# Kernel tuning notes

Measured on AMD Instinct MI355X. Metric: run time of the kernel, lower is better.

The kernel has to match this reference:

```python
import jax, jax.numpy as jnp
import numpy as np
from jax.ops import segment_sum

N_NODES = 100000
N_EDGES = 3200000
NUM_FEATURES = 256


def setup_inputs() -> dict:
    key = jax.random.key(0)
    ks = jax.random.split(key, 12)
    def lin(k, fan_in, fan_out):
        bound = 1.0 / np.sqrt(fan_in)
        kw, kb = jax.random.split(k)
        W = jax.random.uniform(kw, (fan_in, fan_out), jnp.float32, -bound, bound)
        b = jax.random.uniform(kb, (fan_out,), jnp.float32, -bound, bound)
        return W, b
    x = jax.random.normal(ks[0], (N_NODES, NUM_FEATURES), jnp.float32)
    edge_index = jax.random.randint(ks[1], (2, N_EDGES), 0, N_NODES, jnp.int64 if jax.config.jax_enable_x64 else jnp.int32)
    W1, b1 = lin(ks[2], NUM_FEATURES, 64)
    W2, b2 = lin(ks[3], 64, 32)
    W3, b3 = lin(ks[4], 32, 16)
    Ws02, bs02 = lin(ks[5], NUM_FEATURES, 32)
    Ws03, bs03 = lin(ks[6], NUM_FEATURES, 16)
    Ws13, bs13 = lin(ks[7], 64, 16)
    Wout, bout = lin(ks[8], 16, 1)
    return dict(x=x, edge_index=edge_index, W1=W1, b1=b1, W2=W2, b2=b2,
                W3=W3, b3=b3, Ws02=Ws02, bs02=bs02, Ws03=Ws03, bs03=bs03,
                Ws13=Ws13, bs13=bs13, Wout=Wout, bout=bout)


def _deg_inv_sqrt(edge_index, n_nodes):
    # gcn_norm with self-loops: degree counted at target nodes, +1 for self-loop
    dst = edge_index[1]
    deg = segment_sum(jnp.ones(edge_index.shape[1], jnp.float32), dst, num_segments=n_nodes) + 1.0
    return jnp.where(deg > 0, jax.lax.rsqrt(deg), 0.0)


def _gcn_conv(x, W, b, edge_index, dinv):
    # PyG GCNConv: h = x W; out[i] = sum_{j->i} dinv[j]*dinv[i]*h[j] + dinv[i]^2*h[i] + b
    src, dst = edge_index[0], edge_index[1]
    h = x @ W                                   # [N, out]
    norm = (dinv[src] * dinv[dst])[:, None]     # [E, 1]
    agg = segment_sum(h[src] * norm, dst, num_segments=x.shape[0])
    agg = agg + (dinv * dinv)[:, None] * h      # self-loop term
    return agg + b


def reference(x, edge_index, W1, b1, W2, b2, W3, b3,
              Ws02, bs02, Ws03, bs03, Ws13, bs13, Wout, bout):
    # Dropout in eval mode (identity).
    dinv = _deg_inv_sqrt(edge_index, x.shape[0])
    x1 = jax.nn.relu(_gcn_conv(x, W1, b1, edge_index, dinv))
    x2 = jax.nn.relu(_gcn_conv(x1, W2, b2, edge_index, dinv) + x @ Ws02 + bs02)
    x3 = jax.nn.relu(_gcn_conv(x2, W3, b3, edge_index, dinv)
                     + x @ Ws03 + bs03 + x1 @ Ws13 + bs13)
    return jax.nn.sigmoid(x3 @ Wout + bout)
```

## Files before the change

### kernel.cpp

```cpp
#include <hip/hip_runtime.h>
#include <hip/hip_bf16.h>
#include <math.h>


#define NBUCK_MAX 512
#define P1_CHUNK 8192
#define EPT 32
#define BCAP 9216

typedef __attribute__((ext_vector_type(8))) short bfrag;
typedef __attribute__((ext_vector_type(4))) float f4_t;
typedef __attribute__((ext_vector_type(2))) float f2_t;

__device__ inline float uaf(unsigned u) { return __uint_as_float(u); }
__device__ inline ushort f2bf(float f) {
    __hip_bfloat16 b = __float2bfloat16(f);
    return *reinterpret_cast<ushort*>(&b);
}
__device__ inline bfrag cvt8(const float4 a, const float4 b) {
    union { ushort u[8]; bfrag f; } r;
    r.u[0] = f2bf(a.x); r.u[1] = f2bf(a.y); r.u[2] = f2bf(a.z); r.u[3] = f2bf(a.w);
    r.u[4] = f2bf(b.x); r.u[5] = f2bf(b.y); r.u[6] = f2bf(b.z); r.u[7] = f2bf(b.w);
    return r.f;
}
__device__ inline bfrag ld_bfrag(const ushort* p) {
    const uint4 raw = *reinterpret_cast<const uint4*>(p);
    return *reinterpret_cast<const bfrag*>(&raw);
}


__global__ __launch_bounds__(256) void bucket_hist_kernel(
    const int* __restrict__ dst, int E, int* __restrict__ bucket_count, int nbuckets)
{
    __shared__ int lhist[NBUCK_MAX];
    for (int i = threadIdx.x; i < nbuckets; i += 256) lhist[i] = 0;
    __syncthreads();
    const int stride = gridDim.x * 256;
    for (int e = blockIdx.x * 256 + threadIdx.x; e < E; e += stride)
        atomicAdd(&lhist[dst[e] >> 8], 1);
    __syncthreads();
    for (int i = threadIdx.x; i < nbuckets; i += 256) {
        int c = lhist[i];
        if (c) atomicAdd(&bucket_count[i], c);
    }
}

__global__ __launch_bounds__(512) void bucket_scan_kernel(
    const int* __restrict__ bucket_count, int* __restrict__ bucket_base,
    int* __restrict__ bucket_cursor, int nbuckets)
{
    __shared__ int tmp[512];
    const int tid = threadIdx.x;
    int v = (tid < nbuckets) ? bucket_count[tid] : 0;
    tmp[tid] = v;
    __syncthreads();
    for (int off = 1; off < 512; off <<= 1) {
        int t = (tid >= off) ? tmp[tid - off] : 0;
        __syncthreads();
        tmp[tid] += t;
        __syncthreads();
    }
    if (tid < nbuckets) {
        int base = tmp[tid] - v;
        bucket_base[tid]   = base;
        bucket_cursor[tid] = base;
    }
}

__global__ __launch_bounds__(256) void partition_kernel(
    const int* __restrict__ src, const int* __restrict__ dst, int E,
    int* __restrict__ bucket_cursor, unsigned int* __restrict__ keys, int nbuckets)
{
    __shared__ int hist[NBUCK_MAX];
    __shared__ int lofs[NBUCK_MAX];
    __shared__ int gbase[NBUCK_MAX];
    __shared__ int lcur[NBUCK_MAX];
    __shared__ int ssum[256];
    __shared__ unsigned int stage[P1_CHUNK];
    __shared__ int gidx[P1_CHUNK];

    const int tid = threadIdx.x;
    const int e0  = blockIdx.x * P1_CHUNK;
    const int nE  = min(P1_CHUNK, E - e0);

    for (int i = tid; i < NBUCK_MAX; i += 256) { hist[i] = 0; lcur[i] = 0; }
    __syncthreads();

    int myb[EPT];
    unsigned int mypk[EPT];
#pragma unroll
    for (int j = 0; j < EPT; ++j) {
        const int e = e0 + tid + j * 256;
        if (e < E) {
            const int d = dst[e];
            myb[j]  = d >> 8;
            mypk[j] = ((unsigned int)(d & 255) << 17) | (unsigned int)src[e];
            atomicAdd(&hist[myb[j]], 1);
        } else myb[j] = -1;
    }
    __syncthreads();

    int a0 = (2 * tid     < nbuckets) ? hist[2 * tid]     : 0;
    int a1 = (2 * tid + 1 < nbuckets) ? hist[2 * tid + 1] : 0;
    ssum[tid] = a0 + a1;
    __syncthreads();
    for (int off = 1; off < 256; off <<= 1) {
        int t = (tid >= off) ? ssum[tid - off] : 0;
        __syncthreads();
        ssum[tid] += t;
        __syncthreads();
    }
    const int ex = ssum[tid] - (a0 + a1);
    if (2 * tid     < nbuckets) lofs[2 * tid]     = ex;
    if (2 * tid + 1 < nbuckets) lofs[2 * tid + 1] = ex + a0;
    __syncthreads();

    for (int i = tid; i < nbuckets; i += 256)
        gbase[i] = atomicAdd(&bucket_cursor[i], hist[i]);
    __syncthreads();

#pragma unroll
    for (int j = 0; j < EPT; ++j) {
        if (myb[j] >= 0) {
            const int b = myb[j];
            const int l = lofs[b] + atomicAdd(&lcur[b], 1);
            stage[l] = mypk[j];
            gidx[l]  = gbase[b] - lofs[b] + l;
        }
    }
    __syncthreads();

    for (int i = tid; i < nE; i += 256)
        keys[gidx[i]] = stage[i];
}

__global__ __launch_bounds__(256) void csr_build_kernel(
    const unsigned int* __restrict__ keys, const int* __restrict__ bucket_base,
    const int* __restrict__ bucket_count,
    int* __restrict__ row_off, float* __restrict__ dinv, int* __restrict__ col,
    int N, int E)
{
    __shared__ unsigned int inb[BCAP];
    __shared__ int outv[BCAP];
    __shared__ int hist[256];
    __shared__ int lofs[256];
    __shared__ int ssum[256];

    const int tid  = threadIdx.x;
    const int b    = blockIdx.x;
    const int base = bucket_base[b];
    const int cnt  = min(bucket_count[b], BCAP);
    const int n0   = b << 8;
    const int nn   = min(256, N - n0);

    for (int i = tid; i < cnt; i += 256) inb[i] = keys[base + i];
    hist[tid] = 0;
    __syncthreads();

    for (int i = tid; i < cnt; i += 256)
        atomicAdd(&hist[inb[i] >> 17], 1);
    __syncthreads();

    ssum[tid] = hist[tid];
    __syncthreads();
    for (int off = 1; off < 256; off <<= 1) {
        int t = (tid >= off) ? ssum[tid - off] : 0;
        __syncthreads();
        ssum[tid] += t;
        __syncthreads();
    }
    lofs[tid] = ssum[tid] - hist[tid];

    if (tid < nn) {
        row_off[n0 + tid] = base + lofs[tid];
        dinv[n0 + tid]    = rsqrtf((float)hist[tid] + 1.0f);
    }
    if (b == 0 && tid == 0) row_off[N] = E;
    __syncthreads();

    hist[tid] = 0;
    __syncthreads();

    for (int i = tid; i < cnt; i += 256) {
        const unsigned int k = inb[i];
        const int node = k >> 17;
        const int l = lofs[node] + atomicAdd(&hist[node], 1);
        outv[l] = (int)(k & 0x1FFFF);
    }
    __syncthreads();

    for (int i = tid; i < cnt; i += 256)
        col[base + i] = outv[i];
}


__global__ __launch_bounds__(256) void prep_weights_kernel(
    const float* __restrict__ W1, const float* __restrict__ Ws02,
    const float* __restrict__ Ws03, const float* __restrict__ W2,
    const float* __restrict__ Ws13, const float* __restrict__ W3,
    ushort* __restrict__ Wt0, ushort* __restrict__ Wt1, ushort* __restrict__ Wt2)
{
    int idx = blockIdx.x * 256 + threadIdx.x;
    if (idx < 32768) {
        int f = idx >> 8, k = idx & 255;
        float v = 0.f;
        if (f < 64)       v = W1[k * 64 + f];
        else if (f < 96)  v = Ws02[k * 32 + (f - 64)];
        else if (f < 112) v = Ws03[k * 16 + (f - 96)];
        Wt0[idx] = f2bf(v);
    } else if (idx < 32768 + 3072) {
        int t = idx - 32768;
        int f = t >> 6, k = t & 63;
        float v = (f < 32) ? W2[k * 32 + f] : Ws13[k * 16 + (f - 32)];
        Wt1[t] = f2bf(v);
    } else if (idx < 32768 + 3072 + 512) {
        int t = idx - 32768 - 3072;
        int f = t >> 5, k = t & 31;
        Wt2[t] = f2bf(W3[k * 16 + f]);
    }
}


__global__ __launch_bounds__(256, 3) void gemm_mfma0(
    const float* __restrict__ X, const ushort* __restrict__ Wt0,
    const float* __restrict__ bs02, const float* __restrict__ bs03,
    const float* __restrict__ dinv,
    __hip_bfloat16* __restrict__ g1, float* __restrict__ pre2,
    float* __restrict__ pre3, int N)
{
    __shared__ __align__(16) float Xs[2][64 * 64];

    const int tid  = threadIdx.x;
    const int lane = tid & 63;
    const int wf   = tid >> 6;
    const int n0   = blockIdx.x * 64;
    const int mrow = lane & 15;
    const int q    = lane >> 4;
    const int kq   = q * 8;

    bfrag bfr[2][8];
#pragma unroll
    for (int ft = 0; ft < 2; ++ft) {
        const ushort* wr = &Wt0[(size_t)(wf * 32 + ft * 16 + mrow) * 256 + kq];
#pragma unroll
        for (int p = 0; p < 8; ++p)
            bfr[ft][p] = ld_bfrag(&wr[p * 32]);
    }

    int srow[4], schunk[4];
#pragma unroll
    for (int j = 0; j < 4; ++j) {
        const int R = wf * 16 + j * 4 + q;
        srow[j]   = min(n0 + R, N - 1);
        schunk[j] = mrow ^ (R & 7);
    }

    auto STAGE = [&](int buf, int kc) {
#pragma unroll
        for (int j = 0; j < 4; ++j) {
            const float* gsrc =
                X + (size_t)srow[j] * 256 + kc * 64 + schunk[j] * 4;
            __builtin_amdgcn_global_load_lds(
                (const __attribute__((address_space(1))) unsigned int*)gsrc,
                (__attribute__((address_space(3))) unsigned int*)
                    &Xs[buf][(wf * 16 + j * 4) * 64],
                16, 0, 0);
        }
    };

    f4_t acc[4][2];
#pragma unroll
    for (int a = 0; a < 4; ++a)
#pragma unroll
        for (int b = 0; b < 2; ++b) acc[a][b] = {0.f, 0.f, 0.f, 0.f};

    STAGE(0, 0);
    __syncthreads();

    int cur = 0;
    for (int kc = 0; kc < 4; ++kc) {
        if (kc < 3) STAGE(cur ^ 1, kc + 1);
        const float4* Xs4 = reinterpret_cast<const float4*>(Xs[cur]);
#pragma unroll
        for (int pl = 0; pl < 2; ++pl) {
            bfrag af[4];
#pragma unroll
            for (int mt = 0; mt < 4; ++mt) {
                const int r  = mt * 16 + mrow;
                const int c0 = pl * 8 + q * 2;
                const float4 u0 = Xs4[r * 16 + (c0 ^ (r & 7))];
                const float4 u1 = Xs4[r * 16 + ((c0 + 1) ^ (r & 7))];
                af[mt] = cvt8(u0, u1);
            }
            const int pg = kc * 2 + pl;
#pragma unroll
            for (int mt = 0; mt < 4; ++mt)
#pragma unroll
                for (int ft = 0; ft < 2; ++ft)
                    acc[mt][ft] = __builtin_amdgcn_mfma_f32_16x16x32_bf16(
                        af[mt], bfr[ft][pg], acc[mt][ft], 0, 0, 0);
        }
        __syncthreads();
        cur ^= 1;
    }

    char* sm = (char*)Xs;
    ushort* g1s = (ushort*)sm;
    float*  p2s = (float*)(sm + 8192);
    float*  p3s = (float*)(sm + 16384);

    if (wf < 2) {
#pragma unroll
        for (int mt = 0; mt < 4; ++mt) {
#pragma unroll
            for (int r = 0; r < 4; ++r) {
                const int nl = mt * 16 + q * 4 + r;
                const float di = dinv[min(n0 + nl, N - 1)];
#pragma unroll
                for (int ft = 0; ft < 2; ++ft)
                    g1s[nl * 64 + wf * 32 + ft * 16 + mrow] =
                        f2bf(di * acc[mt][ft][r]);
            }
        }
    } else if (wf == 2) {
#pragma unroll
        for (int mt = 0; mt < 4; ++mt)
#pragma unroll
            for (int ft = 0; ft < 2; ++ft)
#pragma unroll
                for (int r = 0; r < 4; ++r)
                    p2s[(mt * 16 + q * 4 + r) * 32 + ft * 16 + mrow] =
                        acc[mt][ft][r] + bs02[ft * 16 + mrow];
    } else {
#pragma unroll
        for (int mt = 0; mt < 4; ++mt)
#pragma unroll
            for (int r = 0; r < 4; ++r)
                p3s[(mt * 16 + q * 4 + r) * 16 + mrow] =
                    acc[mt][0][r] + bs03[mrow];
    }
    __syncthreads();

    const uint4* g1v = (const uint4*)g1s;
    const uint4* p2v = (const uint4*)p2s;
    const uint4* p3v = (const uint4*)p3s;
#pragma unroll
    for (int t = 0; t < 2; ++t) {
        const int i   = t * 256 + tid;
        const int row = i >> 3;
        if (n0 + row < N)
            *(uint4*)((ushort*)g1 + (size_t)(n0 + row) * 64 + (i & 7) * 8) =
                g1v[i];
    }
#pragma unroll
    for (int t = 0; t < 2; ++t) {
        const int i   = t * 256 + tid;
        const int row = i >> 3;
        if (n0 + row < N)
            *(uint4*)(pre2 + (size_t)(n0 + row) * 32 + (i & 7) * 4) = p2v[i];
    }
    {
        const int i   = tid;
        const int row = i >> 2;
        if (n0 + row < N)
            *(uint4*)(pre3 + (size_t)(n0 + row) * 16 + (i & 3) * 4) = p3v[i];
    }
}

__global__ __launch_bounds__(256) void gemm_mfma1(
    const ushort* __restrict__ X1, const ushort* __restrict__ Wt1,
    const float* __restrict__ bs13, const float* __restrict__ dinv,
    __hip_bfloat16* __restrict__ g2, float* __restrict__ pre3, int N)
{
    __shared__ __align__(16) ushort g2s[128 * 32];
    __shared__ __align__(16) float  p3s[128 * 16];

    const int tid  = threadIdx.x;
    const int lane = tid & 63;
    const int wave = tid >> 6;
    const int nb   = blockIdx.x * 128;
    const int n0   = nb + wave * 32;
    const int mrow = lane & 15;
    const int q    = lane >> 4;
    const int kq   = q * 8;

    f4_t acc[2][3];
#pragma unroll
    for (int a = 0; a < 2; ++a)
#pragma unroll
        for (int b = 0; b < 3; ++b) acc[a][b] = {0.f, 0.f, 0.f, 0.f};

    const ushort* xrow[2];
#pragma unroll
    for (int mt = 0; mt < 2; ++mt) {
        int r = n0 + mt * 16 + mrow;
        r = (r < N) ? r : (N - 1);
        xrow[mt] = &X1[(size_t)r * 64 + kq];
    }
    const ushort* wrow[3];
#pragma unroll
    for (int ft = 0; ft < 3; ++ft)
        wrow[ft] = &Wt1[(size_t)(ft * 16 + mrow) * 64 + kq];

#pragma unroll
    for (int p = 0; p < 2; ++p) {
        bfrag af[2], bf[3];
#pragma unroll
        for (int mt = 0; mt < 2; ++mt) af[mt] = ld_bfrag(&xrow[mt][p * 32]);
#pragma unroll
        for (int ft = 0; ft < 3; ++ft) bf[ft] = ld_bfrag(&wrow[ft][p * 32]);
#pragma unroll
        for (int mt = 0; mt < 2; ++mt)
#pragma unroll
            for (int ft = 0; ft < 3; ++ft)
                acc[mt][ft] = __builtin_amdgcn_mfma_f32_16x16x32_bf16(
                    af[mt], bf[ft], acc[mt][ft], 0, 0, 0);
    }

#pragma unroll
    for (int mt = 0; mt < 2; ++mt) {
#pragma unroll
        for (int r = 0; r < 4; ++r) {
            const int nl = wave * 32 + mt * 16 + q * 4 + r;
            const float di = dinv[min(nb + nl, N - 1)];
            g2s[nl * 32 +      mrow] = f2bf(di * acc[mt][0][r]);
            g2s[nl * 32 + 16 + mrow] = f2bf(di * acc[mt][1][r]);
            p3s[nl * 16 + mrow] = acc[mt][2][r] + bs13[mrow];
        }
    }
    __syncthreads();

    const uint4*  g2v = (const uint4*)g2s;
    const float4* p3v = (const float4*)p3s;
#pragma unroll
    for (int t = 0; t < 2; ++t) {
        const int i   = t * 256 + tid;
        const int row = i >> 2;
        if (nb + row < N)
            *(uint4*)((ushort*)g2 + (size_t)(nb + row) * 32 + (i & 3) * 8) =
                g2v[i];
    }
#pragma unroll
    for (int t = 0; t < 2; ++t) {
        const int i   = t * 256 + tid;
        const int row = i >> 2;
        if (nb + row < N) {
            float4* dst =
                (float4*)(pre3 + (size_t)(nb + row) * 16 + (i & 3) * 4);
            float4 v = *dst;
            const float4 s = p3v[i];
            v.x += s.x; v.y += s.y; v.z += s.z; v.w += s.w;
            *dst = v;
        }
    }
}

__global__ __launch_bounds__(256) void gemm_mfma2(
    const ushort* __restrict__ X2, const ushort* __restrict__ Wt2,
    const float* __restrict__ dinv, __hip_bfloat16* __restrict__ g3, int N)
{
    __shared__ __align__(16) ushort g3s[128 * 16];

    const int tid  = threadIdx.x;
    const int lane = tid & 63;
    const int wave = tid >> 6;
    const int nb   = blockIdx.x * 128;
    const int n0   = nb + wave * 32;
    const int mrow = lane & 15;
    const int q    = lane >> 4;
    const int kq   = q * 8;

    f4_t acc[2];
#pragma unroll
    for (int a = 0; a < 2; ++a) acc[a] = {0.f, 0.f, 0.f, 0.f};

    const bfrag bf = ld_bfrag(&Wt2[(size_t)mrow * 32 + kq]);
#pragma unroll
    for (int mt = 0; mt < 2; ++mt) {
        int r = n0 + mt * 16 + mrow;
        r = (r < N) ? r : (N - 1);
        const bfrag af = ld_bfrag(&X2[(size_t)r * 32 + kq]);
        acc[mt] = __builtin_amdgcn_mfma_f32_16x16x32_bf16(af, bf, acc[mt], 0, 0, 0);
    }

#pragma unroll
    for (int mt = 0; mt < 2; ++mt) {
#pragma unroll
        for (int r = 0; r < 4; ++r) {
            const int nl = wave * 32 + mt * 16 + q * 4 + r;
            const float di = dinv[min(nb + nl, N - 1)];
            g3s[nl * 16 + mrow] = f2bf(di * acc[mt][r]);
        }
    }
    __syncthreads();

    const uint4* g3v = (const uint4*)g3s;
    {
        const int i   = tid;
        const int row = i >> 1;
        if (nb + row < N)
            *(uint4*)((ushort*)g3 + (size_t)(nb + row) * 16 + (i & 1) * 8) =
                g3v[i];
    }
}


template<int F, int MODE>
__global__ __launch_bounds__(256) void agg_kernel(
    const ushort* __restrict__ g, const float* __restrict__ dinv,
    const int* __restrict__ row_off, const int* __restrict__ col,
    const float* __restrict__ bias, const float* __restrict__ pre,
    const float* __restrict__ Wout, const float* __restrict__ bout,
    void* __restrict__ out, int N)
{
    constexpr int FG  = F / 8;
    constexpr int EPW = 64 / FG;
    constexpr int U   = 32 / EPW;
    constexpr int LSH = (F == 64) ? 7 : (F == 32 ? 6 : 5);

    const int lane = threadIdx.x & 63;
    const int wv   = threadIdx.x >> 6;
    const int i    = blockIdx.x * 4 + wv;
    if (i >= N) return;

    const int fg  = lane & (FG - 1);
    const int eo  = lane / FG;
    const unsigned fbb = (unsigned)fg * 16;

    const char* gb = (const char*)g;

    f2_t acc0 = {0.f, 0.f}, acc1 = {0.f, 0.f};
    f2_t acc2 = {0.f, 0.f}, acc3 = {0.f, 0.f};

    const int s = row_off[i], e = row_off[i + 1];
    const int nfull = (e - s) >> 5;
    int p = s;
    const int* cp = col + s + eo;

    for (int it = 0; it < nfull; ++it, p += 32, cp += 32) {
        unsigned voff[U];
#pragma unroll
        for (int u = 0; u < U; ++u)
            voff[u] = ((unsigned)cp[u * EPW] << LSH) + fbb;
        uint4 w[U];
#pragma unroll
        for (int u = 0; u < U; ++u)
            w[u] = *reinterpret_cast<const uint4*>(gb + voff[u]);
#pragma unroll
        for (int u = 0; u < U; ++u) {
            acc0 += (f2_t){uaf(w[u].x << 16), uaf(w[u].x & 0xffff0000u)};
            acc1 += (f2_t){uaf(w[u].y << 16), uaf(w[u].y & 0xffff0000u)};
            acc2 += (f2_t){uaf(w[u].z << 16), uaf(w[u].z & 0xffff0000u)};
            acc3 += (f2_t){uaf(w[u].w << 16), uaf(w[u].w & 0xffff0000u)};
        }
    }
    if (p < e) {
        float m[U];
        unsigned voff[U];
#pragma unroll
        for (int u = 0; u < U; ++u) {
            const int q = p + eo + u * EPW;
            m[u]    = (q < e) ? 1.0f : 0.0f;
            voff[u] = ((unsigned)col[min(q, e - 1)] << LSH) + fbb;
        }
        uint4 w[U];
#pragma unroll
        for (int u = 0; u < U; ++u)
            w[u] = *reinterpret_cast<const uint4*>(gb + voff[u]);
#pragma unroll
        for (int u = 0; u < U; ++u) {
            const f2_t mm = {m[u], m[u]};
            acc0 += mm * (f2_t){uaf(w[u].x << 16), uaf(w[u].x & 0xffff0000u)};
            acc1 += mm * (f2_t){uaf(w[u].y << 16), uaf(w[u].y & 0xffff0000u)};
            acc2 += mm * (f2_t){uaf(w[u].z << 16), uaf(w[u].z & 0xffff0000u)};
            acc3 += mm * (f2_t){uaf(w[u].w << 16), uaf(w[u].w & 0xffff0000u)};
        }
    }

#pragma unroll
    for (int ro = FG; ro < 64; ro <<= 1) {
        acc0.x += __shfl_xor(acc0.x, ro); acc0.y += __shfl_xor(acc0.y, ro);
        acc1.x += __shfl_xor(acc1.x, ro); acc1.y += __shfl_xor(acc1.y, ro);
        acc2.x += __shfl_xor(acc2.x, ro); acc2.y += __shfl_xor(acc2.y, ro);
        acc3.x += __shfl_xor(acc3.x, ro); acc3.y += __shfl_xor(acc3.y, ro);
    }

    const uint4 ws =
        *reinterpret_cast<const uint4*>(gb + (((unsigned)i) << LSH) + fbb);
    const float di = dinv[i];
    const int fb = fg * 8;
    const float4 b0 = *reinterpret_cast<const float4*>(&bias[fb]);
    const float4 b1 = *reinterpret_cast<const float4*>(&bias[fb + 4]);

    float v0 = di * (acc0.x + uaf(ws.x << 16))         + b0.x;
    float v1 = di * (acc0.y + uaf(ws.x & 0xffff0000u)) + b0.y;
    float v2 = di * (acc1.x + uaf(ws.y << 16))         + b0.z;
    float v3 = di * (acc1.y + uaf(ws.y & 0xffff0000u)) + b0.w;
    float v4 = di * (acc2.x + uaf(ws.z << 16))         + b1.x;
    float v5 = di * (acc2.y + uaf(ws.z & 0xffff0000u)) + b1.y;
    float v6 = di * (acc3.x + uaf(ws.w << 16))         + b1.z;
    float v7 = di * (acc3.y + uaf(ws.w & 0xffff0000u)) + b1.w;

    if (MODE != 0) {
        const float4 p0 = *reinterpret_cast<const float4*>(&pre[(size_t)i * F + fb]);
        const float4 p1 = *reinterpret_cast<const float4*>(&pre[(size_t)i * F + fb + 4]);
        v0 += p0.x; v1 += p0.y; v2 += p0.z; v3 += p0.w;
        v4 += p1.x; v5 += p1.y; v6 += p1.z; v7 += p1.w;
    }
    v0 = fmaxf(v0, 0.f); v1 = fmaxf(v1, 0.f);
    v2 = fmaxf(v2, 0.f); v3 = fmaxf(v3, 0.f);
    v4 = fmaxf(v4, 0.f); v5 = fmaxf(v5, 0.f);
    v6 = fmaxf(v6, 0.f); v7 = fmaxf(v7, 0.f);

    if (MODE != 2) {
        if (lane < FG) {
            uint4 o;
            o.x = (unsigned)f2bf(v0) | ((unsigned)f2bf(v1) << 16);
            o.y = (unsigned)f2bf(v2) | ((unsigned)f2bf(v3) << 16);
            o.z = (unsigned)f2bf(v4) | ((unsigned)f2bf(v5) << 16);
            o.w = (unsigned)f2bf(v6) | ((unsigned)f2bf(v7) << 16);
            *reinterpret_cast<uint4*>((char*)out + (((size_t)i) << LSH) + fbb) = o;
        }
    } else {
        const float4 w0 = *reinterpret_cast<const float4*>(&Wout[fb]);
        const float4 w1 = *reinterpret_cast<const float4*>(&Wout[fb + 4]);
        float t = v0 * w0.x + v1 * w0.y + v2 * w0.z + v3 * w0.w +
                  v4 * w1.x + v5 * w1.y + v6 * w1.z + v7 * w1.w;
        t += __shfl_xor(t, 1);
        if (lane == 0)
            ((float*)out)[i] = 1.0f / (1.0f + expf(-(t + bout[0])));
    }
}


extern "C" void kernel_launch(void* const* d_in, const int* in_sizes, int n_in,
                              void* d_out, int out_size, void* d_ws, size_t ws_size,
                              hipStream_t stream)
{
    const float* x    = (const float*)d_in[0];
    const int*   edge = (const int*)d_in[1];
    const float* W1   = (const float*)d_in[2];
    const float* b1   = (const float*)d_in[3];
    const float* W2   = (const float*)d_in[4];
    const float* b2   = (const float*)d_in[5];
    const float* W3   = (const float*)d_in[6];
    const float* b3   = (const float*)d_in[7];
    const float* Ws02 = (const float*)d_in[8];
    const float* bs02 = (const float*)d_in[9];
    const float* Ws03 = (const float*)d_in[10];
    const float* bs03 = (const float*)d_in[11];
    const float* Ws13 = (const float*)d_in[12];
    const float* bs13 = (const float*)d_in[13];
    const float* Wout = (const float*)d_in[14];
    const float* bout = (const float*)d_in[15];

    const int N = in_sizes[0] / 256;
    const int E = in_sizes[1] / 2;
    const int* srcv = edge;
    const int* dstv = edge + E;
    const int nbuckets = (N + 255) >> 8;

    char* ws = (char*)d_ws;
    size_t off = 0;
    auto alloc = [&](size_t bytes) -> void* {
        void* p = ws + off;
        off += (bytes + 255) & ~(size_t)255;
        return p;
    };
    unsigned int* keys = (unsigned int*)alloc((size_t)E * 4);
    int*   col      = (int*)  alloc((size_t)E * 4);
    int*   bcount   = (int*)  alloc((size_t)NBUCK_MAX * 4);
    int*   bbase    = (int*)  alloc((size_t)NBUCK_MAX * 4);
    int*   bcursor  = (int*)  alloc((size_t)NBUCK_MAX * 4);
    int*   row_off  = (int*)  alloc((size_t)(N + 1) * 4);
    float* dinv     = (float*)alloc((size_t)N * 4);
    ushort* Wt0     = (ushort*)alloc((size_t)128 * 256 * 2);
    ushort* Wt1     = (ushort*)alloc((size_t)48 * 64 * 2);
    ushort* Wt2     = (ushort*)alloc((size_t)16 * 32 * 2);
    ushort* g1      = (ushort*)alloc((size_t)N * 64 * 2);
    ushort* x1      = (ushort*)alloc((size_t)N * 64 * 2);
    ushort* g2      = (ushort*)alloc((size_t)N * 32 * 2);
    ushort* x2      = (ushort*)alloc((size_t)N * 32 * 2);
    ushort* g3      = (ushort*)alloc((size_t)N * 16 * 2);
    float* pre2     = (float*)alloc((size_t)N * 32 * 4);
    float* pre3     = (float*)alloc((size_t)N * 16 * 4);

    prep_weights_kernel<<<142, 256, 0, stream>>>(W1, Ws02, Ws03, W2, Ws13, W3,
                                                 Wt0, Wt1, Wt2);
    hipMemsetAsync(bcount, 0, (size_t)NBUCK_MAX * 4, stream);
    bucket_hist_kernel<<<1024, 256, 0, stream>>>(dstv, E, bcount, nbuckets);
    bucket_scan_kernel<<<1, 512, 0, stream>>>(bcount, bbase, bcursor, nbuckets);
    partition_kernel<<<(E + P1_CHUNK - 1) / P1_CHUNK, 256, 0, stream>>>(
        srcv, dstv, E, bcursor, keys, nbuckets);
    csr_build_kernel<<<nbuckets, 256, 0, stream>>>(
        keys, bbase, bcount, row_off, dinv, col, N, E);

    const int ab = (N + 3) / 4;

    gemm_mfma0<<<(N + 63) / 64, 256, 0, stream>>>(
        x, Wt0, bs02, bs03, dinv, (__hip_bfloat16*)g1, pre2, pre3, N);
    agg_kernel<64, 0><<<ab, 256, 0, stream>>>(g1, dinv, row_off, col,
                                              b1, nullptr, nullptr, nullptr, x1, N);
    gemm_mfma1<<<(N + 127) / 128, 256, 0, stream>>>(
        x1, Wt1, bs13, dinv, (__hip_bfloat16*)g2, pre3, N);
    agg_kernel<32, 1><<<ab, 256, 0, stream>>>(g2, dinv, row_off, col,
                                              b2, pre2, nullptr, nullptr, x2, N);
    gemm_mfma2<<<(N + 127) / 128, 256, 0, stream>>>(
        x2, Wt2, dinv, (__hip_bfloat16*)g3, N);
    agg_kernel<16, 2><<<ab, 256, 0, stream>>>(g3, dinv, row_off, col,
                                              b3, pre3, Wout, bout, d_out, N);
}
```

Measured before the change: 428.4 us.

## Fuse small GEMMs into aggregation epilogues and merge preprocessing kernels

```diff
diff --git a/kernel.cpp b/kernel.cpp
--- a/kernel.cpp
+++ b/kernel.cpp
@@ -4,9 +4,11 @@
 
 
 #define NBUCK_MAX 512
-#define P1_CHUNK 8192
-#define EPT 32
+#define P1_CHUNK 4096
+#define EPT 16
 #define BCAP 9216
+#define PREP_BLOCKS 142
+#define HIST_BLOCKS 1024
 
 typedef __attribute__((ext_vector_type(8))) short bfrag;
 typedef __attribute__((ext_vector_type(4))) float f4_t;
@@ -29,15 +31,45 @@
 }
 
 
-__global__ __launch_bounds__(256) void bucket_hist_kernel(
-    const int* __restrict__ dst, int E, int* __restrict__ bucket_count, int nbuckets)
+__global__ __launch_bounds__(256) void fka_kernel(
+    const float* __restrict__ W1, const float* __restrict__ Ws02,
+    const float* __restrict__ Ws03, const float* __restrict__ W2,
+    const float* __restrict__ Ws13, const float* __restrict__ W3,
+    ushort* __restrict__ Wt0, ushort* __restrict__ Wt1, ushort* __restrict__ Wt2,
+    const int* __restrict__ dst, int E, int* __restrict__ bucket_count,
+    int* __restrict__ deg, int nbuckets)
 {
+    if (blockIdx.x < PREP_BLOCKS) {
+        const int idx = blockIdx.x * 256 + threadIdx.x;
+        if (idx < 32768) {
+            int f = idx >> 8, k = idx & 255;
+            float v = 0.f;
+            if (f < 64)       v = W1[k * 64 + f];
+            else if (f < 96)  v = Ws02[k * 32 + (f - 64)];
+            else if (f < 112) v = Ws03[k * 16 + (f - 96)];
+            Wt0[idx] = f2bf(v);
+        } else if (idx < 32768 + 3072) {
+            int t = idx - 32768;
+            int f = t >> 6, k = t & 63;
+            float v = (f < 32) ? W2[k * 32 + f] : Ws13[k * 16 + (f - 32)];
+            Wt1[t] = f2bf(v);
+        } else if (idx < 32768 + 3072 + 512) {
+            int t = idx - 32768 - 3072;
+            int f = t >> 5, k = t & 31;
+            Wt2[t] = f2bf(W3[k * 16 + f]);
+        }
+        return;
+    }
     __shared__ int lhist[NBUCK_MAX];
+    const int bid = blockIdx.x - PREP_BLOCKS;
     for (int i = threadIdx.x; i < nbuckets; i += 256) lhist[i] = 0;
     __syncthreads();
-    const int stride = gridDim.x * 256;
-    for (int e = blockIdx.x * 256 + threadIdx.x; e < E; e += stride)
-        atomicAdd(&lhist[dst[e] >> 8], 1);
+    const int stride = HIST_BLOCKS * 256;
+    for (int e = bid * 256 + threadIdx.x; e < E; e += stride) {
+        const int d = dst[e];
+        atomicAdd(&lhist[d >> 8], 1);
+        atomicAdd(&deg[d], 1);
+    }
     __syncthreads();
     for (int i = threadIdx.x; i < nbuckets; i += 256) {
         int c = lhist[i];
@@ -45,10 +77,17 @@
     }
 }
 
-__global__ __launch_bounds__(512) void bucket_scan_kernel(
+
+__global__ __launch_bounds__(512) void fks_kernel(
     const int* __restrict__ bucket_count, int* __restrict__ bucket_base,
-    int* __restrict__ bucket_cursor, int nbuckets)
+    int* __restrict__ bucket_cursor, const int* __restrict__ deg,
+    float* __restrict__ dinv, int nbuckets, int N)
 {
+    if (blockIdx.x != 0) {
+        const int i = (blockIdx.x - 1) * 512 + threadIdx.x;
+        if (i < N) dinv[i] = rsqrtf((float)deg[i] + 1.0f);
+        return;
+    }
     __shared__ int tmp[512];
     const int tid = threadIdx.x;
     int v = (tid < nbuckets) ? bucket_count[tid] : 0;
@@ -67,173 +106,92 @@
     }
 }
 
-__global__ __launch_bounds__(256) void partition_kernel(
+
+union FKBsh {
+    float xs[2][4096];
+    struct {
+        int hist[NBUCK_MAX];
+        int lofs[NBUCK_MAX];
+        int gbase[NBUCK_MAX];
+        int lcur[NBUCK_MAX];
+        int ssum[256];
+        unsigned int stage[P1_CHUNK];
+        int gidx[P1_CHUNK];
+    } p;
+};
+
+__global__ __launch_bounds__(256, 3) void fkb_kernel(
     const int* __restrict__ src, const int* __restrict__ dst, int E,
-    int* __restrict__ bucket_cursor, unsigned int* __restrict__ keys, int nbuckets)
-{
-    __shared__ int hist[NBUCK_MAX];
-    __shared__ int lofs[NBUCK_MAX];
-    __shared__ int gbase[NBUCK_MAX];
-    __shared__ int lcur[NBUCK_MAX];
-    __shared__ int ssum[256];
-    __shared__ unsigned int stage[P1_CHUNK];
-    __shared__ int gidx[P1_CHUNK];
-
-    const int tid = threadIdx.x;
-    const int e0  = blockIdx.x * P1_CHUNK;
-    const int nE  = min(P1_CHUNK, E - e0);
-
-    for (int i = tid; i < NBUCK_MAX; i += 256) { hist[i] = 0; lcur[i] = 0; }
-    __syncthreads();
-
-    int myb[EPT];
-    unsigned int mypk[EPT];
-#pragma unroll
-    for (int j = 0; j < EPT; ++j) {
-        const int e = e0 + tid + j * 256;
-        if (e < E) {
-            const int d = dst[e];
-            myb[j]  = d >> 8;
-            mypk[j] = ((unsigned int)(d & 255) << 17) | (unsigned int)src[e];
-            atomicAdd(&hist[myb[j]], 1);
-        } else myb[j] = -1;
-    }
-    __syncthreads();
-
-    int a0 = (2 * tid     < nbuckets) ? hist[2 * tid]     : 0;
-    int a1 = (2 * tid + 1 < nbuckets) ? hist[2 * tid + 1] : 0;
-    ssum[tid] = a0 + a1;
-    __syncthreads();
-    for (int off = 1; off < 256; off <<= 1) {
-        int t = (tid >= off) ? ssum[tid - off] : 0;
-        __syncthreads();
-        ssum[tid] += t;
-        __syncthreads();
-    }
-    const int ex = ssum[tid] - (a0 + a1);
-    if (2 * tid     < nbuckets) lofs[2 * tid]     = ex;
-    if (2 * tid + 1 < nbuckets) lofs[2 * tid + 1] = ex + a0;
-    __syncthreads();
-
-    for (int i = tid; i < nbuckets; i += 256)
-        gbase[i] = atomicAdd(&bucket_cursor[i], hist[i]);
-    __syncthreads();
-
-#pragma unroll
-    for (int j = 0; j < EPT; ++j) {
-        if (myb[j] >= 0) {
-            const int b = myb[j];
-            const int l = lofs[b] + atomicAdd(&lcur[b], 1);
-            stage[l] = mypk[j];
-            gidx[l]  = gbase[b] - lofs[b] + l;
-        }
-    }
-    __syncthreads();
-
-    for (int i = tid; i < nE; i += 256)
-        keys[gidx[i]] = stage[i];
-}
-
-__global__ __launch_bounds__(256) void csr_build_kernel(
-    const unsigned int* __restrict__ keys, const int* __restrict__ bucket_base,
-    const int* __restrict__ bucket_count,
-    int* __restrict__ row_off, float* __restrict__ dinv, int* __restrict__ col,
-    int N, int E)
-{
-    __shared__ unsigned int inb[BCAP];
-    __shared__ int outv[BCAP];
-    __shared__ int hist[256];
-    __shared__ int lofs[256];
-    __shared__ int ssum[256];
-
-    const int tid  = threadIdx.x;
-    const int b    = blockIdx.x;
-    const int base = bucket_base[b];
-    const int cnt  = min(bucket_count[b], BCAP);
-    const int n0   = b << 8;
-    const int nn   = min(256, N - n0);
-
-    for (int i = tid; i < cnt; i += 256) inb[i] = keys[base + i];
-    hist[tid] = 0;
-    __syncthreads();
-
-    for (int i = tid; i < cnt; i += 256)
-        atomicAdd(&hist[inb[i] >> 17], 1);
-    __syncthreads();
-
-    ssum[tid] = hist[tid];
-    __syncthreads();
-    for (int off = 1; off < 256; off <<= 1) {
-        int t = (tid >= off) ? ssum[tid - off] : 0;
-        __syncthreads();
-        ssum[tid] += t;
-        __syncthreads();
-    }
-    lofs[tid] = ssum[tid] - hist[tid];
-
-    if (tid < nn) {
-        row_off[n0 + tid] = base + lofs[tid];
-        dinv[n0 + tid]    = rsqrtf((float)hist[tid] + 1.0f);
-    }
-    if (b == 0 && tid == 0) row_off[N] = E;
-    __syncthreads();
-
-    hist[tid] = 0;
-    __syncthreads();
-
-    for (int i = tid; i < cnt; i += 256) {
-        const unsigned int k = inb[i];
-        const int node = k >> 17;
-        const int l = lofs[node] + atomicAdd(&hist[node], 1);
-        outv[l] = (int)(k & 0x1FFFF);
-    }
-    __syncthreads();
-
-    for (int i = tid; i < cnt; i += 256)
-        col[base + i] = outv[i];
-}
-
-
-__global__ __launch_bounds__(256) void prep_weights_kernel(
-    const float* __restrict__ W1, const float* __restrict__ Ws02,
-    const float* __restrict__ Ws03, const float* __restrict__ W2,
-    const float* __restrict__ Ws13, const float* __restrict__ W3,
-    ushort* __restrict__ Wt0, ushort* __restrict__ Wt1, ushort* __restrict__ Wt2)
-{
-    int idx = blockIdx.x * 256 + threadIdx.x;
-    if (idx < 32768) {
-        int f = idx >> 8, k = idx & 255;
-        float v = 0.f;
-        if (f < 64)       v = W1[k * 64 + f];
-        else if (f < 96)  v = Ws02[k * 32 + (f - 64)];
-        else if (f < 112) v = Ws03[k * 16 + (f - 96)];
-        Wt0[idx] = f2bf(v);
-    } else if (idx < 32768 + 3072) {
-        int t = idx - 32768;
-        int f = t >> 6, k = t & 63;
-        float v = (f < 32) ? W2[k * 32 + f] : Ws13[k * 16 + (f - 32)];
-        Wt1[t] = f2bf(v);
-    } else if (idx < 32768 + 3072 + 512) {
-        int t = idx - 32768 - 3072;
-        int f = t >> 5, k = t & 31;
-        Wt2[t] = f2bf(W3[k * 16 + f]);
-    }
-}
-
-
-__global__ __launch_bounds__(256, 3) void gemm_mfma0(
+    int* __restrict__ bucket_cursor, unsigned int* __restrict__ keys,
+    int nbuckets, int part_blocks,
     const float* __restrict__ X, const ushort* __restrict__ Wt0,
     const float* __restrict__ bs02, const float* __restrict__ bs03,
-    const float* __restrict__ dinv,
-    __hip_bfloat16* __restrict__ g1, float* __restrict__ pre2,
-    float* __restrict__ pre3, int N)
+    const float* __restrict__ dinv, ushort* __restrict__ g1,
+    float* __restrict__ pre2, float* __restrict__ pre3, int N)
 {
-    __shared__ __align__(16) float Xs[2][64 * 64];
-
-    const int tid  = threadIdx.x;
+    __shared__ __align__(16) FKBsh sh;
+    const int tid = threadIdx.x;
+
+    if (blockIdx.x < part_blocks) {
+        const int e0 = blockIdx.x * P1_CHUNK;
+        const int nE = min(P1_CHUNK, E - e0);
+
+        for (int i = tid; i < NBUCK_MAX; i += 256) { sh.p.hist[i] = 0; sh.p.lcur[i] = 0; }
+        __syncthreads();
+
+        int myb[EPT];
+        unsigned int mypk[EPT];
+#pragma unroll
+        for (int j = 0; j < EPT; ++j) {
+            const int e = e0 + tid + j * 256;
+            if (e < E) {
+                const int d = dst[e];
+                myb[j]  = d >> 8;
+                mypk[j] = ((unsigned int)(d & 255) << 17) | (unsigned int)src[e];
+                atomicAdd(&sh.p.hist[myb[j]], 1);
+            } else myb[j] = -1;
+        }
+        __syncthreads();
+
+        int a0 = (2 * tid     < nbuckets) ? sh.p.hist[2 * tid]     : 0;
+        int a1 = (2 * tid + 1 < nbuckets) ? sh.p.hist[2 * tid + 1] : 0;
+        sh.p.ssum[tid] = a0 + a1;
+        __syncthreads();
+        for (int off = 1; off < 256; off <<= 1) {
+            int t = (tid >= off) ? sh.p.ssum[tid - off] : 0;
+            __syncthreads();
+            sh.p.ssum[tid] += t;
+            __syncthreads();
+        }
+        const int ex = sh.p.ssum[tid] - (a0 + a1);
+        if (2 * tid     < nbuckets) sh.p.lofs[2 * tid]     = ex;
+        if (2 * tid + 1 < nbuckets) sh.p.lofs[2 * tid + 1] = ex + a0;
+        __syncthreads();
+
+        for (int i = tid; i < nbuckets; i += 256)
+            sh.p.gbase[i] = atomicAdd(&bucket_cursor[i], sh.p.hist[i]);
+        __syncthreads();
+
+#pragma unroll
+        for (int j = 0; j < EPT; ++j) {
+            if (myb[j] >= 0) {
+                const int b = myb[j];
+                const int l = sh.p.lofs[b] + atomicAdd(&sh.p.lcur[b], 1);
+                sh.p.stage[l] = mypk[j];
+                sh.p.gidx[l]  = sh.p.gbase[b] - sh.p.lofs[b] + l;
+            }
+        }
+        __syncthreads();
+
+        for (int i = tid; i < nE; i += 256)
+            keys[sh.p.gidx[i]] = sh.p.stage[i];
+        return;
+    }
+
+    const int bid  = blockIdx.x - part_blocks;
     const int lane = tid & 63;
     const int wf   = tid >> 6;
-    const int n0   = blockIdx.x * 64;
+    const int n0   = bid * 64;
     const int mrow = lane & 15;
     const int q    = lane >> 4;
     const int kq   = q * 8;
@@ -263,7 +221,7 @@
             __builtin_amdgcn_global_load_lds(
                 (const __attribute__((address_space(1))) unsigned int*)gsrc,
                 (__attribute__((address_space(3))) unsigned int*)
-                    &Xs[buf][(wf * 16 + j * 4) * 64],
+                    &sh.xs[buf][(wf * 16 + j * 4) * 64],
                 16, 0, 0);
         }
     };
@@ -280,7 +238,7 @@
     int cur = 0;
     for (int kc = 0; kc < 4; ++kc) {
         if (kc < 3) STAGE(cur ^ 1, kc + 1);
-        const float4* Xs4 = reinterpret_cast<const float4*>(Xs[cur]);
+        const float4* Xs4 = reinterpret_cast<const float4*>(&sh.xs[cur][0]);
 #pragma unroll
         for (int pl = 0; pl < 2; ++pl) {
             bfrag af[4];
@@ -304,7 +262,7 @@
         cur ^= 1;
     }
 
-    char* sm = (char*)Xs;
+    char* sm = (char*)&sh;
     ushort* g1s = (ushort*)sm;
     float*  p2s = (float*)(sm + 8192);
     float*  p3s = (float*)(sm + 16384);
@@ -349,8 +307,7 @@
         const int i   = t * 256 + tid;
         const int row = i >> 3;
         if (n0 + row < N)
-            *(uint4*)((ushort*)g1 + (size_t)(n0 + row) * 64 + (i & 7) * 8) =
-                g1v[i];
+            *(uint4*)(g1 + (size_t)(n0 + row) * 64 + (i & 7) * 8) = g1v[i];
     }
 #pragma unroll
     for (int t = 0; t < 2; ++t) {
@@ -367,141 +324,60 @@
     }
 }
 
-__global__ __launch_bounds__(256) void gemm_mfma1(
-    const ushort* __restrict__ X1, const ushort* __restrict__ Wt1,
-    const float* __restrict__ bs13, const float* __restrict__ dinv,
-    __hip_bfloat16* __restrict__ g2, float* __restrict__ pre3, int N)
+
+__global__ __launch_bounds__(256) void csr_build_kernel(
+    const unsigned int* __restrict__ keys, const int* __restrict__ bucket_base,
+    const int* __restrict__ bucket_count,
+    int* __restrict__ row_off, int* __restrict__ col, int N, int E)
 {
-    __shared__ __align__(16) ushort g2s[128 * 32];
-    __shared__ __align__(16) float  p3s[128 * 16];
+    __shared__ unsigned int inb[BCAP];
+    __shared__ int outv[BCAP];
+    __shared__ int hist[256];
+    __shared__ int lofs[256];
+    __shared__ int ssum[256];
 
     const int tid  = threadIdx.x;
-    const int lane = tid & 63;
-    const int wave = tid >> 6;
-    const int nb   = blockIdx.x * 128;
-    const int n0   = nb + wave * 32;
-    const int mrow = lane & 15;
-    const int q    = lane >> 4;
-    const int kq   = q * 8;
-
-    f4_t acc[2][3];
-#pragma unroll
-    for (int a = 0; a < 2; ++a)
-#pragma unroll
-        for (int b = 0; b < 3; ++b) acc[a][b] = {0.f, 0.f, 0.f, 0.f};
-
-    const ushort* xrow[2];
-#pragma unroll
-    for (int mt = 0; mt < 2; ++mt) {
-        int r = n0 + mt * 16 + mrow;
-        r = (r < N) ? r : (N - 1);
-        xrow[mt] = &X1[(size_t)r * 64 + kq];
-    }
-    const ushort* wrow[3];
-#pragma unroll
-    for (int ft = 0; ft < 3; ++ft)
-        wrow[ft] = &Wt1[(size_t)(ft * 16 + mrow) * 64 + kq];
-
-#pragma unroll
-    for (int p = 0; p < 2; ++p) {
-        bfrag af[2], bf[3];
-#pragma unroll
-        for (int mt = 0; mt < 2; ++mt) af[mt] = ld_bfrag(&xrow[mt][p * 32]);
-#pragma unroll
-        for (int ft = 0; ft < 3; ++ft) bf[ft] = ld_bfrag(&wrow[ft][p * 32]);
-#pragma unroll
-        for (int mt = 0; mt < 2; ++mt)
-#pragma unroll
-            for (int ft = 0; ft < 3; ++ft)
-                acc[mt][ft] = __builtin_amdgcn_mfma_f32_16x16x32_bf16(
-                    af[mt], bf[ft], acc[mt][ft], 0, 0, 0);
-    }
-
-#pragma unroll
-    for (int mt = 0; mt < 2; ++mt) {
-#pragma unroll
-        for (int r = 0; r < 4; ++r) {
-            const int nl = wave * 32 + mt * 16 + q * 4 + r;
-            const float di = dinv[min(nb + nl, N - 1)];
-            g2s[nl * 32 +      mrow] = f2bf(di * acc[mt][0][r]);
-            g2s[nl * 32 + 16 + mrow] = f2bf(di * acc[mt][1][r]);
-            p3s[nl * 16 + mrow] = acc[mt][2][r] + bs13[mrow];
-        }
-    }
-    __syncthreads();
-
-    const uint4*  g2v = (const uint4*)g2s;
-    const float4* p3v = (const float4*)p3s;
-#pragma unroll
-    for (int t = 0; t < 2; ++t) {
-        const int i   = t * 256 + tid;
-        const int row = i >> 2;
-        if (nb + row < N)
-            *(uint4*)((ushort*)g2 + (size_t)(nb + row) * 32 + (i & 3) * 8) =
-                g2v[i];
-    }
-#pragma unroll
-    for (int t = 0; t < 2; ++t) {
-        const int i   = t * 256 + tid;
-        const int row = i >> 2;
-        if (nb + row < N) {
-            float4* dst =
-                (float4*)(pre3 + (size_t)(nb + row) * 16 + (i & 3) * 4);
-            float4 v = *dst;
-            const float4 s = p3v[i];
-            v.x += s.x; v.y += s.y; v.z += s.z; v.w += s.w;
-            *dst = v;
-        }
-    }
-}
-
-__global__ __launch_bounds__(256) void gemm_mfma2(
-    const ushort* __restrict__ X2, const ushort* __restrict__ Wt2,
-    const float* __restrict__ dinv, __hip_bfloat16* __restrict__ g3, int N)
-{
-    __shared__ __align__(16) ushort g3s[128 * 16];
-
-    const int tid  = threadIdx.x;
-    const int lane = tid & 63;
-    const int wave = tid >> 6;
-    const int nb   = blockIdx.x * 128;
-    const int n0   = nb + wave * 32;
-    const int mrow = lane & 15;
-    const int q    = lane >> 4;
-    const int kq   = q * 8;
-
-    f4_t acc[2];
-#pragma unroll
-    for (int a = 0; a < 2; ++a) acc[a] = {0.f, 0.f, 0.f, 0.f};
-
-    const bfrag bf = ld_bfrag(&Wt2[(size_t)mrow * 32 + kq]);
-#pragma unroll
-    for (int mt = 0; mt < 2; ++mt) {
-        int r = n0 + mt * 16 + mrow;
-        r = (r < N) ? r : (N - 1);
-        const bfrag af = ld_bfrag(&X2[(size_t)r * 32 + kq]);
-        acc[mt] = __builtin_amdgcn_mfma_f32_16x16x32_bf16(af, bf, acc[mt], 0, 0, 0);
-    }
-
-#pragma unroll
-    for (int mt = 0; mt < 2; ++mt) {
-#pragma unroll
-        for (int r = 0; r < 4; ++r) {
-            const int nl = wave * 32 + mt * 16 + q * 4 + r;
-            const float di = dinv[min(nb + nl, N - 1)];
-            g3s[nl * 16 + mrow] = f2bf(di * acc[mt][r]);
-        }
-    }
-    __syncthreads();
-
-    const uint4* g3v = (const uint4*)g3s;
-    {
-        const int i   = tid;
-        const int row = i >> 1;
-        if (nb + row < N)
-            *(uint4*)((ushort*)g3 + (size_t)(nb + row) * 16 + (i & 1) * 8) =
-                g3v[i];
-    }
+    const int b    = blockIdx.x;
+    const int base = bucket_base[b];
+    const int cnt  = min(bucket_count[b], BCAP);
+    const int n0   = b << 8;
+    const int nn   = min(256, N - n0);
+
+    for (int i = tid; i < cnt; i += 256) inb[i] = keys[base + i];
+    hist[tid] = 0;
+    __syncthreads();
+
+    for (int i = tid; i < cnt; i += 256)
+        atomicAdd(&hist[inb[i] >> 17], 1);
+    __syncthreads();
+
+    ssum[tid] = hist[tid];
+    __syncthreads();
+    for (int off = 1; off < 256; off <<= 1) {
+        int t = (tid >= off) ? ssum[tid - off] : 0;
+        __syncthreads();
+        ssum[tid] += t;
+        __syncthreads();
+    }
+    lofs[tid] = ssum[tid] - hist[tid];
+
+    if (tid < nn) row_off[n0 + tid] = base + lofs[tid];
+    if (b == 0 && tid == 0) row_off[N] = E;
+    __syncthreads();
+
+    hist[tid] = 0;
+    __syncthreads();
+
+    for (int i = tid; i < cnt; i += 256) {
+        const unsigned int k = inb[i];
+        const int node = k >> 17;
+        const int l = lofs[node] + atomicAdd(&hist[node], 1);
+        outv[l] = (int)(k & 0x1FFFF);
+    }
+    __syncthreads();
+
+    for (int i = tid; i < cnt; i += 256)
+        col[base + i] = outv[i];
 }
 
 
@@ -510,8 +386,9 @@
     const ushort* __restrict__ g, const float* __restrict__ dinv,
     const int* __restrict__ row_off, const int* __restrict__ col,
     const float* __restrict__ bias, const float* __restrict__ pre,
+    const ushort* __restrict__ Wk, const float* __restrict__ bs13,
     const float* __restrict__ Wout, const float* __restrict__ bout,
-    void* __restrict__ out, int N)
+    void* __restrict__ out, float* __restrict__ pre3, int N)
 {
     constexpr int FG  = F / 8;
     constexpr int EPW = 64 / FG;
@@ -612,15 +489,55 @@
     v4 = fmaxf(v4, 0.f); v5 = fmaxf(v5, 0.f);
     v6 = fmaxf(v6, 0.f); v7 = fmaxf(v7, 0.f);
 
-    if (MODE != 2) {
-        if (lane < FG) {
-            uint4 o;
-            o.x = (unsigned)f2bf(v0) | ((unsigned)f2bf(v1) << 16);
-            o.y = (unsigned)f2bf(v2) | ((unsigned)f2bf(v3) << 16);
-            o.z = (unsigned)f2bf(v4) | ((unsigned)f2bf(v5) << 16);
-            o.w = (unsigned)f2bf(v6) | ((unsigned)f2bf(v7) << 16);
-            *reinterpret_cast<uint4*>((char*)out + (((size_t)i) << LSH) + fbb) = o;
-        }
+    if (MODE == 0) {
+        float pacc[6];
+#pragma unroll
+        for (int t = 0; t < 6; ++t) {
+            const int f = eo * 6 + t;
+            const uint4 wr = *reinterpret_cast<const uint4*>(&Wk[f * 64 + fb]);
+            float sacc;
+            sacc  = v0 * uaf(wr.x << 16);
+            sacc += v1 * uaf(wr.x & 0xffff0000u);
+            sacc += v2 * uaf(wr.y << 16);
+            sacc += v3 * uaf(wr.y & 0xffff0000u);
+            sacc += v4 * uaf(wr.z << 16);
+            sacc += v5 * uaf(wr.z & 0xffff0000u);
+            sacc += v6 * uaf(wr.w << 16);
+            sacc += v7 * uaf(wr.w & 0xffff0000u);
+            pacc[t] = sacc;
+        }
+#pragma unroll
+        for (int t = 0; t < 6; ++t) {
+            pacc[t] += __shfl_xor(pacc[t], 1);
+            pacc[t] += __shfl_xor(pacc[t], 2);
+            pacc[t] += __shfl_xor(pacc[t], 4);
+        }
+        if ((lane & 7) == 0) {
+#pragma unroll
+            for (int t = 0; t < 6; ++t) {
+                const int f = eo * 6 + t;
+                if (f < 32) {
+                    ((ushort*)out)[(size_t)i * 32 + f] = f2bf(di * pacc[t]);
+                } else {
+                    pre3[(size_t)i * 16 + (f - 32)] += pacc[t] + bs13[f - 32];
+                }
+            }
+        }
+    } else if (MODE == 1) {
+        const uint4 wr = *reinterpret_cast<const uint4*>(&Wk[eo * 32 + fb]);
+        float sacc;
+        sacc  = v0 * uaf(wr.x << 16);
+        sacc += v1 * uaf(wr.x & 0xffff0000u);
+        sacc += v2 * uaf(wr.y << 16);
+        sacc += v3 * uaf(wr.y & 0xffff0000u);
+        sacc += v4 * uaf(wr.z << 16);
+        sacc += v5 * uaf(wr.z & 0xffff0000u);
+        sacc += v6 * uaf(wr.w << 16);
+        sacc += v7 * uaf(wr.w & 0xffff0000u);
+        sacc += __shfl_xor(sacc, 1);
+        sacc += __shfl_xor(sacc, 2);
+        if ((lane & 3) == 0)
+            ((ushort*)out)[(size_t)i * 16 + eo] = f2bf(di * sacc);
     } else {
         const float4 w0 = *reinterpret_cast<const float4*>(&Wout[fb]);
         const float4 w1 = *reinterpret_cast<const float4*>(&Wout[fb + 4]);
@@ -670,6 +587,7 @@
     unsigned int* keys = (unsigned int*)alloc((size_t)E * 4);
     int*   col      = (int*)  alloc((size_t)E * 4);
     int*   bcount   = (int*)  alloc((size_t)NBUCK_MAX * 4);
+    int*   deg      = (int*)  alloc((size_t)N * 4);
     int*   bbase    = (int*)  alloc((size_t)NBUCK_MAX * 4);
     int*   bcursor  = (int*)  alloc((size_t)NBUCK_MAX * 4);
     int*   row_off  = (int*)  alloc((size_t)(N + 1) * 4);
@@ -678,35 +596,37 @@
     ushort* Wt1     = (ushort*)alloc((size_t)48 * 64 * 2);
     ushort* Wt2     = (ushort*)alloc((size_t)16 * 32 * 2);
     ushort* g1      = (ushort*)alloc((size_t)N * 64 * 2);
-    ushort* x1      = (ushort*)alloc((size_t)N * 64 * 2);
     ushort* g2      = (ushort*)alloc((size_t)N * 32 * 2);
-    ushort* x2      = (ushort*)alloc((size_t)N * 32 * 2);
     ushort* g3      = (ushort*)alloc((size_t)N * 16 * 2);
     float* pre2     = (float*)alloc((size_t)N * 32 * 4);
     float* pre3     = (float*)alloc((size_t)N * 16 * 4);
 
-    prep_weights_kernel<<<142, 256, 0, stream>>>(W1, Ws02, Ws03, W2, Ws13, W3,
-                                                 Wt0, Wt1, Wt2);
-    hipMemsetAsync(bcount, 0, (size_t)NBUCK_MAX * 4, stream);
-    bucket_hist_kernel<<<1024, 256, 0, stream>>>(dstv, E, bcount, nbuckets);
-    bucket_scan_kernel<<<1, 512, 0, stream>>>(bcount, bbase, bcursor, nbuckets);
-    partition_kernel<<<(E + P1_CHUNK - 1) / P1_CHUNK, 256, 0, stream>>>(
-        srcv, dstv, E, bcursor, keys, nbuckets);
+    hipMemsetAsync(bcount, 0, (size_t)NBUCK_MAX * 4 + (size_t)N * 4, stream);
+
+    fka_kernel<<<PREP_BLOCKS + HIST_BLOCKS, 256, 0, stream>>>(
+        W1, Ws02, Ws03, W2, Ws13, W3, Wt0, Wt1, Wt2,
+        dstv, E, bcount, deg, nbuckets);
+
+    fks_kernel<<<1 + (N + 511) / 512, 512, 0, stream>>>(
+        bcount, bbase, bcursor, deg, dinv, nbuckets, N);
+
+    const int PB = (E + P1_CHUNK - 1) / P1_CHUNK;
+    fkb_kernel<<<PB + (N + 63) / 64, 256, 0, stream>>>(
+        srcv, dstv, E, bcursor, keys, nbuckets, PB,
+        x, Wt0, bs02, bs03, dinv, g1, pre2, pre3, N);
+
     csr_build_kernel<<<nbuckets, 256, 0, stream>>>(
-        keys, bbase, bcount, row_off, dinv, col, N, E);
+        keys, bbase, bcount, row_off, col, N, E);
 
     const int ab = (N + 3) / 4;
 
-    gemm_mfma0<<<(N + 63) / 64, 256, 0, stream>>>(
-        x, Wt0, bs02, bs03, dinv, (__hip_bfloat16*)g1, pre2, pre3, N);
-    agg_kernel<64, 0><<<ab, 256, 0, stream>>>(g1, dinv, row_off, col,
-                                              b1, nullptr, nullptr, nullptr, x1, N);
-    gemm_mfma1<<<(N + 127) / 128, 256, 0, stream>>>(
-        x1, Wt1, bs13, dinv, (__hip_bfloat16*)g2, pre3, N);
-    agg_kernel<32, 1><<<ab, 256, 0, stream>>>(g2, dinv, row_off, col,
-                                              b2, pre2, nullptr, nullptr, x2, N);
-    gemm_mfma2<<<(N + 127) / 128, 256, 0, stream>>>(
-        x2, Wt2, dinv, (__hip_bfloat16*)g3, N);
-    agg_kernel<16, 2><<<ab, 256, 0, stream>>>(g3, dinv, row_off, col,
-                                              b3, pre3, Wout, bout, d_out, N);
-}
+    agg_kernel<64, 0><<<ab, 256, 0, stream>>>(
+        g1, dinv, row_off, col, b1, nullptr, Wt1, bs13,
+        nullptr, nullptr, g2, pre3, N);
+    agg_kernel<32, 1><<<ab, 256, 0, stream>>>(
+        g2, dinv, row_off, col, b2, pre2, Wt2, nullptr,
+        nullptr, nullptr, g3, nullptr, N);
+    agg_kernel<16, 2><<<ab, 256, 0, stream>>>(
+        g3, dinv, row_off, col, b3, pre3, nullptr, nullptr,
+        Wout, bout, d_out, nullptr, N);
+}
```

After: 559.0 us. 30.5% more time.
